# Kernel tuning notes

Measured on AMD Instinct MI355X. Metric: run time of the kernel, lower is better.

Reference implementation:

```python
import jax, jax.numpy as jnp
import numpy as np

VOCAB, EMB, HID, LAYERS, OUT = 50257, 512, 512, 2, 2
B, T = 32, 2048


def setup_inputs() -> dict:
    key = jax.random.key(0)
    ks = jax.random.split(key, 8)
    tokens = jax.random.randint(ks[0], (B, T), 0, VOCAB)
    s = 0.02
    embedding = jax.random.normal(ks[1], (VOCAB, EMB), dtype=jnp.float32) * s
    # per-layer LSTM cell params, gate order (i, f, g, o), stacked over layers
    w_ih = jax.random.normal(ks[2], (LAYERS, 4 * HID, EMB), dtype=jnp.float32) * s
    w_hh = jax.random.normal(ks[3], (LAYERS, 4 * HID, HID), dtype=jnp.float32) * s
    b_ih = jax.random.normal(ks[4], (LAYERS, 4 * HID), dtype=jnp.float32) * s
    b_hh = jax.random.normal(ks[5], (LAYERS, 4 * HID), dtype=jnp.float32) * s
    fc_w = jax.random.normal(ks[6], (OUT, HID), dtype=jnp.float32) * s
    fc_b = jax.random.normal(ks[7], (OUT,), dtype=jnp.float32) * s
    return {"tokens": tokens, "embedding": embedding, "w_ih": w_ih, "w_hh": w_hh,
            "b_ih": b_ih, "b_hh": b_hh, "fc_w": fc_w, "fc_b": fc_b}


def _lstm_forward(tokens, embedding, w_ih, w_hh, b_ih, b_hh, fc_w, fc_b):
    x = embedding[tokens]                       # [B, T, E]
    L = w_ih.shape[0]
    H = w_hh.shape[-1]
    Bsz = tokens.shape[0]
    h0 = jnp.zeros((L, Bsz, H), dtype=x.dtype)
    c0 = jnp.zeros((L, Bsz, H), dtype=x.dtype)

    def step(carry, x_t):                       # x_t: [B, E]
        h, c = carry
        inp = x_t
        hs, cs = [], []
        for l in range(L):
            gates = inp @ w_ih[l].T + b_ih[l] + h[l] @ w_hh[l].T + b_hh[l]  # [B, 4H]
            i, f, g, o = jnp.split(gates, 4, axis=-1)
            c_l = jax.nn.sigmoid(f) * c[l] + jax.nn.sigmoid(i) * jnp.tanh(g)
            h_l = jax.nn.sigmoid(o) * jnp.tanh(c_l)
            hs.append(h_l)
            cs.append(c_l)
            inp = h_l
        return (jnp.stack(hs), jnp.stack(cs)), None

    (h_fin, _), _ = jax.lax.scan(step, (h0, c0), jnp.swapaxes(x, 0, 1))
    out = h_fin[-1]                             # last timestep, top layer: [B, H]
    return jax.nn.sigmoid(out @ fc_w.T + fc_b)  # [B, OUT]


def reference(tokens, embedding, w_ih, w_hh, b_ih, b_hh, fc_w, fc_b):
    return _lstm_forward(tokens, embedding, w_ih, w_hh, b_ih, b_hh, fc_w, fc_b)
```

## Files before the change

### kernel.cpp

```cpp
#include <hip/hip_runtime.h>

#define SEQ   2048
#define EMBD  512
#define HID   512
#define NB    32
#define NSL   128
#define NWG   256
#define NTHR  256

typedef __attribute__((ext_vector_type(8))) short bf16x8;
typedef __attribute__((ext_vector_type(4))) float f32x4;

__device__ __forceinline__ float sigf(float x) { return 1.0f / (1.0f + __expf(-x)); }
__device__ __forceinline__ float tanhf_fast(float x) {
    float e = __expf(2.0f * x);
    return (e - 1.0f) / (e + 1.0f);
}
__device__ __forceinline__ short f2bf(float f) {
    unsigned u = __float_as_uint(f);
    unsigned r = (u + 0x7FFFu + ((u >> 16) & 1u)) >> 16;
    return (short)r;
}
__device__ __forceinline__ float bf2f(unsigned short s) {
    return __uint_as_float(((unsigned)s) << 16);
}
__device__ __forceinline__ unsigned pack2(float a, float b) {
    return (unsigned)(unsigned short)f2bf(a) | ((unsigned)(unsigned short)f2bf(b) << 16);
}
__device__ __forceinline__ bf16x8 cvt8(float4 a, float4 b) {
    bf16x8 r;
    r[0] = f2bf(a.x); r[1] = f2bf(a.y); r[2] = f2bf(a.z); r[3] = f2bf(a.w);
    r[4] = f2bf(b.x); r[5] = f2bf(b.y); r[6] = f2bf(b.z); r[7] = f2bf(b.w);
    return r;
}

__global__ __launch_bounds__(NTHR, 1) void repack_w(
    const float* __restrict__ w_ih, const float* __restrict__ w_hh,
    bf16x8* __restrict__ wsW)
{
    const int wg  = blockIdx.x, tid = threadIdx.x;
    const bool l1 = (wg >= NSL);
    const int s   = l1 ? (wg - NSL) : wg;
    const int layer = l1 ? 1 : 0;
    const int w = tid >> 6, lane = tid & 63, i16 = lane & 15, hi = lane >> 4;
    const int kb = (w & 1) * 256;
    const bool xw = (w < 2);
    const int gg_ = i16 >> 2, jj_ = i16 & 3;
    const int rowg = gg_ * 512 + s * 4 + jj_;
    const float* wbase = xw ? (w_ih + ((size_t)layer * 2048 + rowg) * 512)
                            : (w_hh + ((size_t)layer * 2048 + rowg) * 512);
    #pragma unroll
    for (int q = 0; q < 8; ++q) {
        int koff = kb + q * 32 + hi * 8;
        wsW[(((size_t)wg * 4 + w) * 8 + q) * 64 + lane] =
            cvt8(*(const float4*)(wbase + koff), *(const float4*)(wbase + koff + 4));
    }
}

__global__ __launch_bounds__(NTHR, 1) void lstm_step(
    int k,
    const int*   __restrict__ tokens, const float* __restrict__ emb,
    const bf16x8* __restrict__ wsW,
    const float* __restrict__ b_ih,   const float* __restrict__ b_hh,
    unsigned* __restrict__ hbuf, float* __restrict__ cbuf)
{
    __shared__ float part[8][16][16];

    const int wg  = blockIdx.x, tid = threadIdx.x;
    const bool l1 = (wg >= NSL);
    const int s   = l1 ? (wg - NSL) : wg;
    const int layer = l1 ? 1 : 0;
    const int t = l1 ? (k - 1) : k;
    if (t < 0 || t >= SEQ) return;
    const int p = t & 1;

    const int w = tid >> 6, lane = tid & 63, i16 = lane & 15, hi = lane >> 4;
    const int kb = (w & 1) * 256;
    const bool xw = (w < 2);

    unsigned* const h0a_ = hbuf;
    unsigned* const h0b_ = hbuf + 8192;
    unsigned* const h1a_ = hbuf + 16384;
    unsigned* const h1b_ = hbuf + 24576;

    bf16x8 A[8];
    const bf16x8* wp = wsW + (((size_t)wg * 4 + w) * 8) * 64 + lane;
    #pragma unroll
    for (int q = 0; q < 8; ++q) A[q] = wp[q * 64];

    const unsigned* bsrc;
    if (!l1) bsrc = xw ? (const unsigned*)nullptr : (p ? h0a_ : h0b_);
    else     bsrc = xw ? (p ? h0b_ : h0a_) : (p ? h1a_ : h1b_);

    f32x4 acc0 = {0.f, 0.f, 0.f, 0.f};
    f32x4 acc1 = {0.f, 0.f, 0.f, 0.f};

    if (bsrc == nullptr) {
        const int b0 = i16, b1 = 16 + i16;
        const size_t r0 = (size_t)tokens[b0 * SEQ + t] * EMBD;
        const size_t r1 = (size_t)tokens[b1 * SEQ + t] * EMBD;
        #pragma unroll
        for (int q = 0; q < 8; ++q) {
            int koff = kb + q * 32 + hi * 8;
            float4 xa0 = *(const float4*)(emb + r0 + koff);
            float4 xb0 = *(const float4*)(emb + r0 + koff + 4);
            float4 xa1 = *(const float4*)(emb + r1 + koff);
            float4 xb1 = *(const float4*)(emb + r1 + koff + 4);
            bf16x8 B0 = cvt8(xa0, xb0);
            bf16x8 B1 = cvt8(xa1, xb1);
            acc0 = __builtin_amdgcn_mfma_f32_16x16x32_bf16(A[q], B0, acc0, 0, 0, 0);
            acc1 = __builtin_amdgcn_mfma_f32_16x16x32_bf16(A[q], B1, acc1, 0, 0, 0);
        }
    } else {
        const unsigned* pb0 = bsrc + (size_t)i16 * 256;
        const unsigned* pb1 = bsrc + (size_t)(16 + i16) * 256;
        const int kb2 = kb / 2;
        #pragma unroll
        for (int q = 0; q < 8; ++q) {
            int ko2 = kb2 + q * 16 + hi * 4;
            bf16x8 B0 = *(const bf16x8*)(pb0 + ko2);
            bf16x8 B1 = *(const bf16x8*)(pb1 + ko2);
            acc0 = __builtin_amdgcn_mfma_f32_16x16x32_bf16(A[q], B0, acc0, 0, 0, 0);
            acc1 = __builtin_amdgcn_mfma_f32_16x16x32_bf16(A[q], B1, acc1, 0, 0, 0);
        }
    }

    #pragma unroll
    for (int r = 0; r < 4; ++r) {
        part[w * 2 + 0][hi * 4 + r][i16] = acc0[r];
        part[w * 2 + 1][hi * 4 + r][i16] = acc1[r];
    }
    __syncthreads();

    if (tid < 64) {
        const int eb = tid & 31, pr = tid >> 5;
        const int ect = eb >> 4, ec = eb & 15;
        float gA[4], gB[4];
        #pragma unroll
        for (int g = 0; g < 4; ++g) {
            const int mm = g * 4 + pr * 2;
            const int rg = g * 512 + s * 4 + pr * 2;
            const float bA = b_ih[layer * 2048 + rg]     + b_hh[layer * 2048 + rg];
            const float bB = b_ih[layer * 2048 + rg + 1] + b_hh[layer * 2048 + rg + 1];
            gA[g] = part[0 + ect][mm][ec]     + part[2 + ect][mm][ec]
                  + part[4 + ect][mm][ec]     + part[6 + ect][mm][ec]     + bA;
            gB[g] = part[0 + ect][mm + 1][ec] + part[2 + ect][mm + 1][ec]
                  + part[4 + ect][mm + 1][ec] + part[6 + ect][mm + 1][ec] + bB;
        }
        float* cp = cbuf + (layer ? 16384 : 0) + eb * 512 + s * 4 + pr * 2;
        float2 c2 = *(float2*)cp;
        const float cA = sigf(gA[1]) * c2.x + sigf(gA[0]) * tanhf_fast(gA[2]);
        const float hA = sigf(gA[3]) * tanhf_fast(cA);
        const float cB = sigf(gB[1]) * c2.y + sigf(gB[0]) * tanhf_fast(gB[2]);
        const float hB = sigf(gB[3]) * tanhf_fast(cB);
        *(float2*)cp = make_float2(cA, cB);
        unsigned* hout = l1 ? (p ? h1b_ : h1a_) : (p ? h0b_ : h0a_);
        hout[eb * 256 + s * 2 + pr] = pack2(hA, hB);
    }
}

__global__ void fc_head(const unsigned* __restrict__ h1fin,
                        const float* __restrict__ fc_w,
                        const float* __restrict__ fc_b,
                        float* __restrict__ out)
{
    const int tid = threadIdx.x;
    if (tid >= 64) return;
    const int b = tid >> 1, o = tid & 1;
    float acc = 0.f;
    for (int j2 = 0; j2 < 256; ++j2) {
        unsigned u = h1fin[b * 256 + j2];
        acc += bf2f((unsigned short)(u & 0xFFFFu)) * fc_w[o * HID + 2 * j2]
             + bf2f((unsigned short)(u >> 16))     * fc_w[o * HID + 2 * j2 + 1];
    }
    out[b * 2 + o] = sigf(acc + fc_b[o]);
}

extern "C" void kernel_launch(void* const* d_in, const int* in_sizes, int n_in,
                              void* d_out, int out_size, void* d_ws, size_t ws_size,
                              hipStream_t stream)
{
    const int*   tokens = (const int*)d_in[0];
    const float* emb    = (const float*)d_in[1];
    const float* w_ih   = (const float*)d_in[2];
    const float* w_hh   = (const float*)d_in[3];
    const float* b_ih   = (const float*)d_in[4];
    const float* b_hh   = (const float*)d_in[5];
    const float* fc_w   = (const float*)d_in[6];
    const float* fc_b   = (const float*)d_in[7];

    unsigned* hbuf = (unsigned*)((char*)d_ws + 65536);
    float*    cbuf = (float*)((char*)d_ws + 65536 + 131072);
    bf16x8*   wsW  = (bf16x8*)((char*)d_ws + 65536 + 262144);

    hipMemsetAsync((char*)d_ws + 65536, 0, 262144, stream);
    repack_w<<<dim3(NWG), dim3(NTHR), 0, stream>>>(w_ih, w_hh, wsW);

    for (int k = 0; k <= SEQ; ++k)
        lstm_step<<<dim3(NWG), dim3(NTHR), 0, stream>>>(
            k, tokens, emb, wsW, b_ih, b_hh, hbuf, cbuf);

    fc_head<<<dim3(1), dim3(64), 0, stream>>>(hbuf + 24576, fc_w, fc_b, (float*)d_out);
}
```

Before: 12.17 ms.

## Split each LSTM step over batch halves and precompute transposed tokens and biases

Each per-timestep launch now uses 512 workgroups instead of 256. Every role is split into two batch halves of 16, so each wave does one MFMA chain rather than two. Token indices are transposed once so that per-step token reads are contiguous, and the two bias vectors are summed ahead of time into a workspace buffer. The hidden state is now stored as plain bf16 elements rather than packed pairs. The aim is to shorten each step's critical path and spread work across more CUs, at the cost of loading the weight fragments twice as often per step.

After: 10.66 ms. 1.14x faster.

```diff
diff --git a/kernel.cpp b/kernel.cpp
--- a/kernel.cpp
+++ b/kernel.cpp
@@ -3,9 +3,7 @@
 #define SEQ   2048
 #define EMBD  512
 #define HID   512
-#define NB    32
 #define NSL   128
-#define NWG   256
 #define NTHR  256
 
 typedef __attribute__((ext_vector_type(8))) short bf16x8;
@@ -24,9 +22,6 @@
 __device__ __forceinline__ float bf2f(unsigned short s) {
     return __uint_as_float(((unsigned)s) << 16);
 }
-__device__ __forceinline__ unsigned pack2(float a, float b) {
-    return (unsigned)(unsigned short)f2bf(a) | ((unsigned)(unsigned short)f2bf(b) << 16);
-}
 __device__ __forceinline__ bf16x8 cvt8(float4 a, float4 b) {
     bf16x8 r;
     r[0] = f2bf(a.x); r[1] = f2bf(a.y); r[2] = f2bf(a.z); r[3] = f2bf(a.w);
@@ -38,9 +33,9 @@
     const float* __restrict__ w_ih, const float* __restrict__ w_hh,
     bf16x8* __restrict__ wsW)
 {
-    const int wg  = blockIdx.x, tid = threadIdx.x;
-    const bool l1 = (wg >= NSL);
-    const int s   = l1 ? (wg - NSL) : wg;
+    const int role = blockIdx.x, tid = threadIdx.x;
+    const bool l1 = (role >= NSL);
+    const int s   = l1 ? (role - NSL) : role;
     const int layer = l1 ? 1 : 0;
     const int w = tid >> 6, lane = tid & 63, i16 = lane & 15, hi = lane >> 4;
     const int kb = (w & 1) * 256;
@@ -52,23 +47,37 @@
     #pragma unroll
     for (int q = 0; q < 8; ++q) {
         int koff = kb + q * 32 + hi * 8;
-        wsW[(((size_t)wg * 4 + w) * 8 + q) * 64 + lane] =
+        wsW[(((size_t)role * 4 + w) * 8 + q) * 64 + lane] =
             cvt8(*(const float4*)(wbase + koff), *(const float4*)(wbase + koff + 4));
     }
 }
 
+__global__ void tok_t(const int* __restrict__ tokens, int* __restrict__ tokT)
+{
+    const int idx = blockIdx.x * NTHR + threadIdx.x;
+    const int t = idx >> 5, b = idx & 31;
+    tokT[idx] = tokens[b * SEQ + t];
+}
+
+__global__ void bias_prep(const float* __restrict__ b_ih, const float* __restrict__ b_hh,
+                          float* __restrict__ wsB)
+{
+    const int idx = blockIdx.x * NTHR + threadIdx.x;
+    wsB[idx] = b_ih[idx] + b_hh[idx];
+}
+
 __global__ __launch_bounds__(NTHR, 1) void lstm_step(
     int k,
-    const int*   __restrict__ tokens, const float* __restrict__ emb,
-    const bf16x8* __restrict__ wsW,
-    const float* __restrict__ b_ih,   const float* __restrict__ b_hh,
-    unsigned* __restrict__ hbuf, float* __restrict__ cbuf)
+    const int*   __restrict__ tokT, const float* __restrict__ emb,
+    const bf16x8* __restrict__ wsW, const float* __restrict__ wsB,
+    unsigned short* __restrict__ h16, float* __restrict__ cbuf)
 {
-    __shared__ float part[8][16][16];
+    __shared__ float part[4][16][16];
 
     const int wg  = blockIdx.x, tid = threadIdx.x;
-    const bool l1 = (wg >= NSL);
-    const int s   = l1 ? (wg - NSL) : wg;
+    const int role = wg >> 1, bo = (wg & 1) << 4;
+    const bool l1 = (role >= NSL);
+    const int s   = l1 ? (role - NSL) : role;
     const int layer = l1 ? 1 : 0;
     const int t = l1 ? (k - 1) : k;
     if (t < 0 || t >= SEQ) return;
@@ -78,88 +87,63 @@
     const int kb = (w & 1) * 256;
     const bool xw = (w < 2);
 
-    unsigned* const h0a_ = hbuf;
-    unsigned* const h0b_ = hbuf + 8192;
-    unsigned* const h1a_ = hbuf + 16384;
-    unsigned* const h1b_ = hbuf + 24576;
+    unsigned short* const h0a_ = h16;
+    unsigned short* const h0b_ = h16 + 16384;
+    unsigned short* const h1a_ = h16 + 32768;
+    unsigned short* const h1b_ = h16 + 49152;
 
     bf16x8 A[8];
-    const bf16x8* wp = wsW + (((size_t)wg * 4 + w) * 8) * 64 + lane;
+    const bf16x8* wp = wsW + (((size_t)role * 4 + w) * 8) * 64 + lane;
     #pragma unroll
     for (int q = 0; q < 8; ++q) A[q] = wp[q * 64];
 
-    const unsigned* bsrc;
-    if (!l1) bsrc = xw ? (const unsigned*)nullptr : (p ? h0a_ : h0b_);
+    const unsigned short* bsrc;
+    if (!l1) bsrc = xw ? (const unsigned short*)nullptr : (p ? h0a_ : h0b_);
     else     bsrc = xw ? (p ? h0b_ : h0a_) : (p ? h1a_ : h1b_);
 
-    f32x4 acc0 = {0.f, 0.f, 0.f, 0.f};
-    f32x4 acc1 = {0.f, 0.f, 0.f, 0.f};
+    f32x4 acc = {0.f, 0.f, 0.f, 0.f};
 
     if (bsrc == nullptr) {
-        const int b0 = i16, b1 = 16 + i16;
-        const size_t r0 = (size_t)tokens[b0 * SEQ + t] * EMBD;
-        const size_t r1 = (size_t)tokens[b1 * SEQ + t] * EMBD;
+        const size_t r0 = (size_t)tokT[t * 32 + bo + i16] * EMBD;
         #pragma unroll
         for (int q = 0; q < 8; ++q) {
             int koff = kb + q * 32 + hi * 8;
-            float4 xa0 = *(const float4*)(emb + r0 + koff);
-            float4 xb0 = *(const float4*)(emb + r0 + koff + 4);
-            float4 xa1 = *(const float4*)(emb + r1 + koff);
-            float4 xb1 = *(const float4*)(emb + r1 + koff + 4);
-            bf16x8 B0 = cvt8(xa0, xb0);
-            bf16x8 B1 = cvt8(xa1, xb1);
-            acc0 = __builtin_amdgcn_mfma_f32_16x16x32_bf16(A[q], B0, acc0, 0, 0, 0);
-            acc1 = __builtin_amdgcn_mfma_f32_16x16x32_bf16(A[q], B1, acc1, 0, 0, 0);
+            float4 xa = *(const float4*)(emb + r0 + koff);
+            float4 xb = *(const float4*)(emb + r0 + koff + 4);
+            acc = __builtin_amdgcn_mfma_f32_16x16x32_bf16(A[q], cvt8(xa, xb), acc, 0, 0, 0);
         }
     } else {
-        const unsigned* pb0 = bsrc + (size_t)i16 * 256;
-        const unsigned* pb1 = bsrc + (size_t)(16 + i16) * 256;
-        const int kb2 = kb / 2;
+        const unsigned short* pb = bsrc + (size_t)(bo + i16) * 512 + kb;
         #pragma unroll
         for (int q = 0; q < 8; ++q) {
-            int ko2 = kb2 + q * 16 + hi * 4;
-            bf16x8 B0 = *(const bf16x8*)(pb0 + ko2);
-            bf16x8 B1 = *(const bf16x8*)(pb1 + ko2);
-            acc0 = __builtin_amdgcn_mfma_f32_16x16x32_bf16(A[q], B0, acc0, 0, 0, 0);
-            acc1 = __builtin_amdgcn_mfma_f32_16x16x32_bf16(A[q], B1, acc1, 0, 0, 0);
+            bf16x8 B = *(const bf16x8*)(pb + q * 32 + hi * 8);
+            acc = __builtin_amdgcn_mfma_f32_16x16x32_bf16(A[q], B, acc, 0, 0, 0);
         }
     }
 
     #pragma unroll
-    for (int r = 0; r < 4; ++r) {
-        part[w * 2 + 0][hi * 4 + r][i16] = acc0[r];
-        part[w * 2 + 1][hi * 4 + r][i16] = acc1[r];
-    }
+    for (int r = 0; r < 4; ++r) part[w][hi * 4 + r][i16] = acc[r];
     __syncthreads();
 
     if (tid < 64) {
-        const int eb = tid & 31, pr = tid >> 5;
-        const int ect = eb >> 4, ec = eb & 15;
-        float gA[4], gB[4];
+        const int jj = tid >> 4, bb = tid & 15, eb = bo + bb;
+        float g4[4];
         #pragma unroll
-        for (int g = 0; g < 4; ++g) {
-            const int mm = g * 4 + pr * 2;
-            const int rg = g * 512 + s * 4 + pr * 2;
-            const float bA = b_ih[layer * 2048 + rg]     + b_hh[layer * 2048 + rg];
-            const float bB = b_ih[layer * 2048 + rg + 1] + b_hh[layer * 2048 + rg + 1];
-            gA[g] = part[0 + ect][mm][ec]     + part[2 + ect][mm][ec]
-                  + part[4 + ect][mm][ec]     + part[6 + ect][mm][ec]     + bA;
-            gB[g] = part[0 + ect][mm + 1][ec] + part[2 + ect][mm + 1][ec]
-                  + part[4 + ect][mm + 1][ec] + part[6 + ect][mm + 1][ec] + bB;
-        }
-        float* cp = cbuf + (layer ? 16384 : 0) + eb * 512 + s * 4 + pr * 2;
-        float2 c2 = *(float2*)cp;
-        const float cA = sigf(gA[1]) * c2.x + sigf(gA[0]) * tanhf_fast(gA[2]);
-        const float hA = sigf(gA[3]) * tanhf_fast(cA);
-        const float cB = sigf(gB[1]) * c2.y + sigf(gB[0]) * tanhf_fast(gB[2]);
-        const float hB = sigf(gB[3]) * tanhf_fast(cB);
-        *(float2*)cp = make_float2(cA, cB);
-        unsigned* hout = l1 ? (p ? h1b_ : h1a_) : (p ? h0b_ : h0a_);
-        hout[eb * 256 + s * 2 + pr] = pack2(hA, hB);
+        for (int g = 0; g < 4; ++g)
+            g4[g] = part[0][g * 4 + jj][bb] + part[1][g * 4 + jj][bb]
+                  + part[2][g * 4 + jj][bb] + part[3][g * 4 + jj][bb]
+                  + wsB[layer * 2048 + g * 512 + s * 4 + jj];
+        float* cp = cbuf + layer * 16384 + eb * 512 + s * 4 + jj;
+        float c = *cp;
+        c = sigf(g4[1]) * c + sigf(g4[0]) * tanhf_fast(g4[2]);
+        const float h = sigf(g4[3]) * tanhf_fast(c);
+        *cp = c;
+        unsigned short* hout = l1 ? (p ? h1b_ : h1a_) : (p ? h0b_ : h0a_);
+        hout[eb * 512 + s * 4 + jj] = (unsigned short)f2bf(h);
     }
 }
 
-__global__ void fc_head(const unsigned* __restrict__ h1fin,
+__global__ void fc_head(const unsigned short* __restrict__ h1fin,
                         const float* __restrict__ fc_w,
                         const float* __restrict__ fc_b,
                         float* __restrict__ out)
@@ -168,11 +152,8 @@
     if (tid >= 64) return;
     const int b = tid >> 1, o = tid & 1;
     float acc = 0.f;
-    for (int j2 = 0; j2 < 256; ++j2) {
-        unsigned u = h1fin[b * 256 + j2];
-        acc += bf2f((unsigned short)(u & 0xFFFFu)) * fc_w[o * HID + 2 * j2]
-             + bf2f((unsigned short)(u >> 16))     * fc_w[o * HID + 2 * j2 + 1];
-    }
+    for (int j = 0; j < HID; ++j)
+        acc += bf2f(h1fin[b * 512 + j]) * fc_w[o * HID + j];
     out[b * 2 + o] = sigf(acc + fc_b[o]);
 }
 
@@ -189,16 +170,20 @@
     const float* fc_w   = (const float*)d_in[6];
     const float* fc_b   = (const float*)d_in[7];
 
-    unsigned* hbuf = (unsigned*)((char*)d_ws + 65536);
-    float*    cbuf = (float*)((char*)d_ws + 65536 + 131072);
-    bf16x8*   wsW  = (bf16x8*)((char*)d_ws + 65536 + 262144);
+    float*          wsB  = (float*)d_ws;
+    unsigned short* h16  = (unsigned short*)((char*)d_ws + 65536);
+    float*          cbuf = (float*)((char*)d_ws + 196608);
+    int*            tokT = (int*)((char*)d_ws + 327680);
+    bf16x8*         wsW  = (bf16x8*)((char*)d_ws + 589824);
 
     hipMemsetAsync((char*)d_ws + 65536, 0, 262144, stream);
-    repack_w<<<dim3(NWG), dim3(NTHR), 0, stream>>>(w_ih, w_hh, wsW);
+    tok_t    <<<dim3(256), dim3(NTHR), 0, stream>>>(tokens, tokT);
+    bias_prep<<<dim3(16),  dim3(NTHR), 0, stream>>>(b_ih, b_hh, wsB);
+    repack_w <<<dim3(256), dim3(NTHR), 0, stream>>>(w_ih, w_hh, wsW);
 
     for (int k = 0; k <= SEQ; ++k)
-        lstm_step<<<dim3(NWG), dim3(NTHR), 0, stream>>>(
-            k, tokens, emb, wsW, b_ih, b_hh, hbuf, cbuf);
+        lstm_step<<<dim3(512), dim3(NTHR), 0, stream>>>(
+            k, tokT, emb, wsW, wsB, h16, cbuf);
 
-    fc_head<<<dim3(1), dim3(64), 0, stream>>>(hbuf + 24576, fc_w, fc_b, (float*)d_out);
+    fc_head<<<dim3(1), dim3(64), 0, stream>>>(h16 + 49152, fc_w, fc_b, (float*)d_out);
 }
```
